# Kernel tuning notes

Measured on AMD Instinct MI355X. Metric: run time of the kernel, lower is better.

## Reference

```python
import jax, jax.numpy as jnp
import numpy as np

C = 1.0          # curvature args.c
ALPHA = 3.0      # self.alpha
MIN = 1e-15      # min_norm clamp (HGCN PoincareBall)
PROJ_EPS = 4e-3  # fp32 boundary eps (HGCN)


def _norm(x):
    return jnp.maximum(jnp.linalg.norm(x, axis=-1, keepdims=True), MIN)


def artanh(x):
    # clamp for fp32 stability (HGCN clamps to 1 - 1e-15; 1e-7 is the fp32 analogue)
    return jnp.arctanh(jnp.clip(x, -1.0 + 1e-7, 1.0 - 1e-7))


def proj(x, c):
    n = _norm(x)
    maxn = (1.0 - PROJ_EPS) / jnp.sqrt(c)
    return jnp.where(n > maxn, x / n * maxn, x)


def expmap0(u, c):
    sc = jnp.sqrt(c)
    n = _norm(u)
    return jnp.tanh(sc * n) * u / (sc * n)


def logmap0(p, c):
    sc = jnp.sqrt(c)
    n = _norm(p)
    return artanh(sc * n) * p / (sc * n)


def mobius_add(x, y, c):
    x2 = jnp.sum(x * x, axis=-1, keepdims=True)
    y2 = jnp.sum(y * y, axis=-1, keepdims=True)
    xy = jnp.sum(x * y, axis=-1, keepdims=True)
    num = (1.0 + 2.0 * c * xy + c * y2) * x + (1.0 - c * x2) * y
    den = 1.0 + 2.0 * c * xy + c * c * x2 * y2
    return num / jnp.maximum(den, MIN)


def mobius_matvec(m, x, c):
    sc = jnp.sqrt(c)
    xn = _norm(x)
    mx = x @ m.T                      # [..., out]
    mxn = _norm(mx)
    res = jnp.tanh(mxn / xn * artanh(sc * xn)) * mx / (mxn * sc)
    zero_rows = jnp.all(mx == 0.0, axis=-1, keepdims=True)
    return jnp.where(zero_rows, 0.0, res)


def hyp_linear(x, W, b, c):
    # dropout on weights is identity in eval mode
    mv = proj(mobius_matvec(W, x, c), c)
    hb = proj(expmap0(b[None, :], c), c)  # proj_tan0 is identity on Poincare ball
    return proj(mobius_add(mv, hb, c), c)


def setup_inputs() -> dict:
    key = jax.random.key(0)
    N, D, F = 8192, 128, 128
    ks = jax.random.split(key, 8)
    gain = np.sqrt(2.0 / (D + D)) * np.sqrt(2.0)  # xavier-like scale
    return {
        "idx": jnp.arange(N, dtype=jnp.int32),
        "dist_metrix": jnp.zeros((1,), dtype=jnp.float32),
        "x": jax.random.normal(ks[0], (N, F), dtype=jnp.float32),
        "emb1": jax.random.normal(ks[1], (N, D), dtype=jnp.float32),
        "emb2": jax.random.normal(ks[2], (N, D), dtype=jnp.float32),
        "W1": jax.random.normal(ks[3], (D, D), dtype=jnp.float32) * gain,
        "b1": jax.random.normal(ks[4], (D,), dtype=jnp.float32) * 0.01,
        "W2": jax.random.normal(ks[5], (D, D), dtype=jnp.float32) * gain,
        "b2": jax.random.normal(ks[6], (D,), dtype=jnp.float32) * 0.01,
    }


def reference(idx, dist_metrix, x, emb1, emb2, W1, b1, W2, b2):
    # node embeddings lifted to the Poincare ball (proj_tan0 is identity)
    nv1 = proj(expmap0(emb1[idx], C), C)
    nv2 = proj(expmap0(emb2[idx], C), C)
    nv1 = hyp_linear(nv1, W1, b1, C)
    nv2 = hyp_linear(nv2, W2, b2, C)
    # adjacency construction: a1 = nv2 @ nv1^T (mobius), a2 = nv1 @ nv2^T (mobius)
    a1 = mobius_matvec(nv1, nv2, C)   # [N, N]
    a2 = mobius_matvec(nv2, nv1, C)   # [N, N]
    a = mobius_add(a1, -a2, C)
    adj = jax.nn.relu(jnp.tanh(ALPHA * a))
    n = adj.shape[0]
    adj = adj + 1e-4 * jnp.eye(n, dtype=adj.dtype)
    # row-normalize (scipy round-trip in original == row-sum divide, inf -> 0)
    rs = jnp.sum(adj, axis=1, keepdims=True)
    adj = adj * jnp.where(rs == 0.0, 0.0, 1.0 / rs)
    # propagate features
    xt = logmap0(x, C)                       # [N, F]
    out = mobius_matvec(xt.T, adj, C)        # adj @ xt -> [N, F]
    out = logmap0(out, C)
    return out
```

## Files before the change

### kernel.cpp

```cpp
#include <hip/hip_runtime.h>
#include <hip/hip_bf16.h>


typedef __attribute__((ext_vector_type(8))) short short8;
typedef __attribute__((ext_vector_type(4))) float f32x4;

#define MAXN 0.996f

__device__ __forceinline__ float artanh_clip(float x) {
    x = fminf(x, 1.0f - 1e-7f);
    x = fmaxf(x, -1.0f + 1e-7f);
    return 0.5f * logf((1.0f + x) / (1.0f - x));
}

__device__ __forceinline__ float red8(float v) {
    v += __shfl_xor(v, 1);
    v += __shfl_xor(v, 2);
    v += __shfl_xor(v, 4);
    return v;
}

__device__ __forceinline__ float red64(float v) {
#pragma unroll
    for (int m = 1; m < 64; m <<= 1) v += __shfl_xor(v, m);
    return v;
}

__device__ __forceinline__ unsigned short f2bf(float f) {
    __hip_bfloat16 h = __float2bfloat16(f);
    return *reinterpret_cast<unsigned short*>(&h);
}

__device__ __forceinline__ float bf2f(unsigned short u) {
    __hip_bfloat16 h;
    *reinterpret_cast<unsigned short*>(&h) = u;
    return __bfloat162float(h);
}

__global__ __launch_bounds__(256) void prep_kernel(
    const int* __restrict__ idx, const float* __restrict__ x,
    const float* __restrict__ emb1, const float* __restrict__ emb2,
    const float* __restrict__ W1, const float* __restrict__ W2,
    const float* __restrict__ b1, const float* __restrict__ b2,
    unsigned short* __restrict__ nv1b, unsigned short* __restrict__ nv2b,
    unsigned short* __restrict__ xtT,
    float* __restrict__ xn1, float* __restrict__ xn2) {
    const int which = blockIdx.y;
    const int tid = threadIdx.x;
    const int rblk = blockIdx.x * 32;

    if (which == 2) {
        __shared__ float xv[32 * 132];
        const int r = tid >> 3, s = tid & 7;
        float ev[16];
        float p2 = 0.f;
#pragma unroll
        for (int kk = 0; kk < 16; ++kk) {
            float e = x[(rblk + r) * 128 + s + kk * 8];
            ev[kk] = e;
            p2 += e * e;
        }
        const float n = fmaxf(sqrtf(red8(p2)), 1e-15f);
        const float scl = artanh_clip(n) / n;
#pragma unroll
        for (int kk = 0; kk < 16; ++kk) xv[r * 132 + s + kk * 8] = ev[kk] * scl;
        __syncthreads();
        const int k = tid >> 1, h = tid & 1;
        short8 o0, o1;
#pragma unroll
        for (int j = 0; j < 8; ++j) o0[j] = (short)f2bf(xv[(h * 16 + j) * 132 + k]);
#pragma unroll
        for (int j = 0; j < 8; ++j) o1[j] = (short)f2bf(xv[(h * 16 + 8 + j) * 132 + k]);
        *reinterpret_cast<short8*>(&xtT[k * 8192 + rblk + h * 16]) = o0;
        *reinterpret_cast<short8*>(&xtT[k * 8192 + rblk + h * 16 + 8]) = o1;
        return;
    }

    __shared__ __align__(16) float uL[32 * 132];
    __shared__ float mxL[32 * 132];
    __shared__ float xnL[32];
    __shared__ float hbL[128];
    __shared__ float s2s[4];

    const float* emb = which ? emb2 : emb1;
    const float* W = which ? W2 : W1;
    const float* b = which ? b2 : b1;
    unsigned short* nvb = which ? nv2b : nv1b;
    float* xno = which ? xn2 : xn1;

    float bv = (tid < 128) ? b[tid] : 0.f;
    float ssq = red64(bv * bv);
    if ((tid & 63) == 0) s2s[tid >> 6] = ssq;
    __syncthreads();
    const float bn = fmaxf(sqrtf(s2s[0] + s2s[1]), 1e-15f);
    const float bth = tanhf(bn);
    const float bnu = fmaxf(bth, 1e-15f);
    const float bps = (bnu > MAXN) ? (MAXN / bnu) : 1.0f;
    if (tid < 128) hbL[tid] = bv * (bth / bn) * bps;
    const float hbn = fminf(bnu, MAXN);
    const float y2 = hbn * hbn;

    const int r = tid >> 3, s = tid & 7;
    const int row = rblk + r;
    const int src = idx[row];
    float ev[16];
    float p2 = 0.f;
#pragma unroll
    for (int kk = 0; kk < 16; ++kk) {
        float e = emb[src * 128 + s + kk * 8];
        ev[kk] = e;
        p2 += e * e;
    }
    float n2 = red8(p2);
    float n = fmaxf(sqrtf(n2), 1e-15f);
    float th = tanhf(n);
    float nu = fmaxf(th, 1e-15f);
    float ps = (nu > MAXN) ? (MAXN / nu) : 1.0f;
    float sc0 = (th / n) * ps;
#pragma unroll
    for (int kk = 0; kk < 16; ++kk) uL[r * 132 + s + kk * 8] = ev[kk] * sc0;
    if (s == 0) xnL[r] = fmaxf(nu * ps, 1e-15f);
    __syncthreads();

    const int o = tid & 127, rb = tid >> 7;
    float mxv[16];
#pragma unroll
    for (int rr = 0; rr < 16; ++rr) mxv[rr] = 0.f;
    for (int k4 = 0; k4 < 128; k4 += 4) {
        const float4 wv = *reinterpret_cast<const float4*>(&W[o * 128 + k4]);
#pragma unroll
        for (int rr = 0; rr < 16; ++rr) {
            const float4 uv = *reinterpret_cast<const float4*>(&uL[(rb + rr * 2) * 132 + k4]);
            mxv[rr] += uv.x * wv.x + uv.y * wv.y + uv.z * wv.z + uv.w * wv.w;
        }
    }
#pragma unroll
    for (int rr = 0; rr < 16; ++rr) mxL[(rb + rr * 2) * 132 + o] = mxv[rr];
    __syncthreads();

    float mx[16];
    float m2 = 0.f;
#pragma unroll
    for (int kk = 0; kk < 16; ++kk) {
        mx[kk] = mxL[r * 132 + s + kk * 8];
        m2 += mx[kk] * mx[kk];
    }
    float mxn = fmaxf(sqrtf(red8(m2)), 1e-15f);
    float xnv = xnL[r];
    float tt = tanhf(mxn / xnv * artanh_clip(xnv));
    float nres = fmaxf(tt, 1e-15f);
    float ps2 = (nres > MAXN) ? (MAXN / nres) : 1.0f;
    float s2 = (tt / mxn) * ps2;
    float mvn = nres * ps2;
    float x2 = mvn * mvn;
    float xyp = 0.f;
    float mv[16];
#pragma unroll
    for (int kk = 0; kk < 16; ++kk) {
        mv[kk] = mx[kk] * s2;
        xyp += mv[kk] * hbL[s + kk * 8];
    }
    float xy = red8(xyp);
    float cA = 1.f + 2.f * xy + y2;
    float cB = 1.f - x2;
    float rden = 1.f / fmaxf(1.f + 2.f * xy + x2 * y2, 1e-15f);
    float r2v[16];
    float q2 = 0.f;
#pragma unroll
    for (int kk = 0; kk < 16; ++kk) {
        float v = (cA * mv[kk] + cB * hbL[s + kk * 8]) * rden;
        r2v[kk] = v;
        q2 += v * v;
    }
    float nr2 = fmaxf(sqrtf(red8(q2)), 1e-15f);
    float ps3 = (nr2 > MAXN) ? (MAXN / nr2) : 1.0f;
#pragma unroll
    for (int kk = 0; kk < 16; ++kk) nvb[row * 128 + s + kk * 8] = f2bf(r2v[kk] * ps3);
    if (s == 0) xno[row] = fmaxf((nr2 > MAXN) ? MAXN : nr2, 1e-15f);
}

__global__ __launch_bounds__(256) void gram_kernel(const unsigned short* __restrict__ nv1b,
                                                   const unsigned short* __restrict__ nv2b,
                                                   float* __restrict__ G) {
    __shared__ float Ab[64 * 33], Bb[64 * 33];
    const int tile = blockIdx.x, mat = blockIdx.y, kc = blockIdx.z;
    const int ta = (tile & 3) * 32, tb = (tile >> 2) * 32;
    const unsigned short* Am = (mat == 1) ? nv2b : nv1b;
    const unsigned short* Bm = (mat == 0) ? nv1b : nv2b;
    const int tid = threadIdx.x;
    const int oa = tid & 31, obb = (tid >> 5) * 4;
    float acc[4] = {0.f, 0.f, 0.f, 0.f};
    for (int sc = 0; sc < 16; ++sc) {
        const int r0 = kc * 1024 + sc * 64;
        for (int i0 = tid; i0 < 2048; i0 += 256) {
            int rr = i0 >> 5, cc = i0 & 31;
            Ab[rr * 33 + cc] = bf2f(Am[(r0 + rr) * 128 + ta + cc]);
            Bb[rr * 33 + cc] = bf2f(Bm[(r0 + rr) * 128 + tb + cc]);
        }
        __syncthreads();
#pragma unroll 4
        for (int rr = 0; rr < 64; ++rr) {
            float av = Ab[rr * 33 + oa];
#pragma unroll
            for (int i = 0; i < 4; ++i) acc[i] += av * Bb[rr * 33 + obb + i];
        }
        __syncthreads();
    }
#pragma unroll
    for (int i = 0; i < 4; ++i)
        atomicAdd(&G[mat * 16384 + (ta + oa) * 128 + tb + obb + i], acc[i]);
}

__global__ __launch_bounds__(256) void rowcoef_kernel(
    const float* __restrict__ G, const float* __restrict__ xn1, const float* __restrict__ xn2,
    const unsigned short* __restrict__ nv1b, const unsigned short* __restrict__ nv2b,
    float* __restrict__ P, float* __restrict__ Q) {
    __shared__ __align__(16) float v1L[32 * 132];
    __shared__ __align__(16) float v2L[32 * 132];
    __shared__ float tL[32 * 132];
    __shared__ float RCX[3][32];
    const int tid = threadIdx.x;
    const int rblk = blockIdx.x * 32;
    for (int i = tid; i < 4096; i += 256) {
        int r = i >> 7, c = i & 127;
        v1L[r * 132 + c] = bf2f(nv1b[(rblk + r) * 128 + c]);
        v2L[r * 132 + c] = bf2f(nv2b[(rblk + r) * 128 + c]);
    }
    __syncthreads();
    const int o = tid & 127, rb = tid >> 7;
    const int rA = tid >> 3, sA = tid & 7;
    for (int mat = 0; mat < 3; ++mat) {
        const float* vR = (mat == 0) ? v2L : v1L;
        const float* vL = (mat == 1) ? v1L : v2L;
        const float* Gm = G + mat * 16384;
        float tv[16];
#pragma unroll
        for (int rr = 0; rr < 16; ++rr) tv[rr] = 0.f;
        for (int k4 = 0; k4 < 128; k4 += 4) {
            const float4 gv = *reinterpret_cast<const float4*>(&Gm[o * 128 + k4]);
#pragma unroll
            for (int rr = 0; rr < 16; ++rr) {
                const float4 uv = *reinterpret_cast<const float4*>(&vR[(rb + rr * 2) * 132 + k4]);
                tv[rr] += uv.x * gv.x + uv.y * gv.y + uv.z * gv.z + uv.w * gv.w;
            }
        }
        __syncthreads();
#pragma unroll
        for (int rr = 0; rr < 16; ++rr) {
            int rw = rb + rr * 2;
            tL[rw * 132 + o] = vL[rw * 132 + o] * tv[rr];
        }
        __syncthreads();
        float p = 0.f;
#pragma unroll
        for (int kk = 0; kk < 16; ++kk) p += tL[rA * 132 + sA + kk * 8];
        p = red8(p);
        if (sA == 0) RCX[mat][rA] = p;
    }
    __syncthreads();
    if (tid < 32) {
        const int row = rblk + tid;
        const float R = RCX[0][tid], Cc = RCX[1][tid], X = RCX[2][tid];
        const float xn1v = xn1[row], xn2v = xn2[row];
        const float mxn1 = fmaxf(sqrtf(fmaxf(R, 0.f)), 1e-15f);
        const float t1 = tanhf(mxn1 / xn2v * artanh_clip(xn2v));
        const float f1 = t1 / mxn1;
        const float mxn2 = fmaxf(sqrtf(fmaxf(Cc, 0.f)), 1e-15f);
        const float t2 = tanhf(mxn2 / xn1v * artanh_clip(xn1v));
        const float f2 = t2 / mxn2;
        const float x2 = f1 * f1 * R, y2 = f2 * f2 * Cc;
        const float xy = -f1 * f2 * X;
        const float rden = 1.f / fmaxf(1.f + 2.f * xy + x2 * y2, 1e-15f);
        P[row] = (1.f + 2.f * xy + y2) * f1 * rden;
        Q[row] = -(1.f - x2) * f2 * rden;
    }
}

__global__ __launch_bounds__(512) void fused_kernel(
    const unsigned short* __restrict__ nv1b, const unsigned short* __restrict__ nv2b,
    const unsigned short* __restrict__ xtT,
    const float* __restrict__ P, const float* __restrict__ Q,
    float* __restrict__ out) {
    __shared__ float UL[32 * 132];
    __shared__ float rsL[32], qL[32];

    const int tid = threadIdx.x;
    const int w = tid >> 6, l = tid & 63;
    const int g = l >> 4, c = l & 15;
    const int i0 = blockIdx.x * 32;

    for (int i = tid; i < 32 * 132; i += 512) UL[i] = 0.f;
    if (tid < 32) { rsL[tid] = 0.f; qL[tid] = 0.f; }
    __syncthreads();

    const float Pv0 = P[i0 + c], Pv1 = P[i0 + 16 + c];
    const float Qv0 = Q[i0 + c], Qv1 = Q[i0 + 16 + c];
    const bool needS2 = __any((fabsf(Qv0) > 1e-6f) || (fabsf(Qv1) > 1e-6f)) != 0;

    short8 Bn0[4], Bn1[4];
#pragma unroll
    for (int kk = 0; kk < 4; ++kk) {
        Bn0[kk] = *reinterpret_cast<const short8*>(nv2b + (i0 + c) * 128 + kk * 32 + g * 8);
        Bn1[kk] = *reinterpret_cast<const short8*>(nv2b + (i0 + 16 + c) * 128 + kk * 32 + g * 8);
    }

    const f32x4 z4 = {0.f, 0.f, 0.f, 0.f};
    f32x4 accU0[8], accU1[8];
#pragma unroll
    for (int ft = 0; ft < 8; ++ft) { accU0[ft] = z4; accU1[ft] = z4; }
    float rs0 = 0.f, rs1 = 0.f, q0 = 0.f, q1 = 0.f;

    const int aoff = (8 * (c >> 2) + (c & 3)) * 128 + g * 8;
    const int sdiag = i0 >> 5;
    const int tdiag = ((sdiag & 7) == w) ? (sdiag >> 3) : -1;
    const size_t xoff = (size_t)c * 8192 + g * 8;

    auto elem = [&](float s, float s2v, float Pv, float Qv, int jglob, int iglob,
                    bool dd, float& rsa, float& qa) -> float {
        float a = Pv * s;
        if (needS2) a = fmaf(Qv, s2v, a);
        float e = __builtin_amdgcn_exp2f(a * 8.65617025f);
        float t = 1.0f - 2.0f * __builtin_amdgcn_rcpf(e + 1.0f);
        float ad = fmaxf(t, 0.0f);
        if (dd && (jglob == iglob)) ad += 1e-4f;
        rsa += ad;
        qa = fmaf(ad, ad, qa);
        return ad;
    };
    auto pack8 = [](const float* ad) -> short8 {
        union { unsigned u[4]; short8 s; } r;
#pragma unroll
        for (int k = 0; k < 4; ++k)
            r.u[k] = (unsigned)f2bf(ad[2 * k]) | ((unsigned)f2bf(ad[2 * k + 1]) << 16);
        return r.s;
    };

    auto doStep = [&](int jb, bool dd) __attribute__((always_inline)) {
        const unsigned short* pa = nv1b + (size_t)jb * 128;
        short8 A0[4], A1[4];
#pragma unroll
        for (int kk = 0; kk < 4; ++kk) {
            A0[kk] = *reinterpret_cast<const short8*>(pa + aoff + kk * 32);
            A1[kk] = *reinterpret_cast<const short8*>(pa + aoff + 512 + kk * 32);
        }
        f32x4 s00 = z4, s10 = z4, s01 = z4, s11 = z4;
#pragma unroll
        for (int kk = 0; kk < 4; ++kk) {
            s00 = __builtin_amdgcn_mfma_f32_16x16x32_bf16(A0[kk], Bn0[kk], s00, 0, 0, 0);
            s10 = __builtin_amdgcn_mfma_f32_16x16x32_bf16(A1[kk], Bn0[kk], s10, 0, 0, 0);
            s01 = __builtin_amdgcn_mfma_f32_16x16x32_bf16(A0[kk], Bn1[kk], s01, 0, 0, 0);
            s11 = __builtin_amdgcn_mfma_f32_16x16x32_bf16(A1[kk], Bn1[kk], s11, 0, 0, 0);
        }
        f32x4 r00 = z4, r10 = z4, r01 = z4, r11 = z4;
        if (needS2) {
            const unsigned short* pa2 = nv2b + (size_t)jb * 128;
            short8 C0[4], C1[4], D0[4], D1[4];
#pragma unroll
            for (int kk = 0; kk < 4; ++kk) {
                C0[kk] = *reinterpret_cast<const short8*>(pa2 + aoff + kk * 32);
                C1[kk] = *reinterpret_cast<const short8*>(pa2 + aoff + 512 + kk * 32);
                D0[kk] = *reinterpret_cast<const short8*>(nv1b + (i0 + c) * 128 + kk * 32 + g * 8);
                D1[kk] = *reinterpret_cast<const short8*>(nv1b + (i0 + 16 + c) * 128 + kk * 32 + g * 8);
            }
#pragma unroll
            for (int kk = 0; kk < 4; ++kk) {
                r00 = __builtin_amdgcn_mfma_f32_16x16x32_bf16(C0[kk], D0[kk], r00, 0, 0, 0);
                r10 = __builtin_amdgcn_mfma_f32_16x16x32_bf16(C1[kk], D0[kk], r10, 0, 0, 0);
                r01 = __builtin_amdgcn_mfma_f32_16x16x32_bf16(C0[kk], D1[kk], r01, 0, 0, 0);
                r11 = __builtin_amdgcn_mfma_f32_16x16x32_bf16(C1[kk], D1[kk], r11, 0, 0, 0);
            }
        }
        float ad0[8], ad1[8];
        const int jg = jb + 8 * g;
        const int ig0 = i0 + c, ig1 = i0 + 16 + c;
#pragma unroll
        for (int v = 0; v < 4; ++v) {
            ad0[v]     = elem(s00[v], r00[v], Pv0, Qv0, jg + v,     ig0, dd, rs0, q0);
            ad0[4 + v] = elem(s10[v], r10[v], Pv0, Qv0, jg + 4 + v, ig0, dd, rs0, q0);
            ad1[v]     = elem(s01[v], r01[v], Pv1, Qv1, jg + v,     ig1, dd, rs1, q1);
            ad1[4 + v] = elem(s11[v], r11[v], Pv1, Qv1, jg + 4 + v, ig1, dd, rs1, q1);
        }
        const short8 af0 = pack8(ad0);
        const short8 af1 = pack8(ad1);
#pragma unroll
        for (int ft = 0; ft < 8; ++ft) {
            short8 xb = *reinterpret_cast<const short8*>(xtT + (size_t)ft * 16 * 8192 + xoff + jb);
            accU0[ft] = __builtin_amdgcn_mfma_f32_16x16x32_bf16(af0, xb, accU0[ft], 0, 0, 0);
            accU1[ft] = __builtin_amdgcn_mfma_f32_16x16x32_bf16(af1, xb, accU1[ft], 0, 0, 0);
        }
    };

    for (int t = 0; t < 32; ++t) {
        const int jb = (w + 8 * t) * 32;
        if (t == tdiag) doStep(jb, true);
        else doStep(jb, false);
    }

    rs0 += __shfl_xor(rs0, 16); rs0 += __shfl_xor(rs0, 32);
    rs1 += __shfl_xor(rs1, 16); rs1 += __shfl_xor(rs1, 32);
    q0 += __shfl_xor(q0, 16);   q0 += __shfl_xor(q0, 32);
    q1 += __shfl_xor(q1, 16);   q1 += __shfl_xor(q1, 32);
    if (l < 16) {
        atomicAdd(&rsL[c], rs0);
        atomicAdd(&qL[c], q0);
        atomicAdd(&rsL[16 + c], rs1);
        atomicAdd(&qL[16 + c], q1);
    }
#pragma unroll
    for (int ft = 0; ft < 8; ++ft)
#pragma unroll
        for (int v = 0; v < 4; ++v) {
            atomicAdd(&UL[(4 * g + v) * 132 + ft * 16 + c], accU0[ft][v]);
            atomicAdd(&UL[(16 + 4 * g + v) * 132 + ft * 16 + c], accU1[ft][v]);
        }
    __syncthreads();

    const int r = tid >> 4, cc = tid & 15;
    const float rsv = rsL[r];
    const float wv = (rsv == 0.f) ? 0.f : 1.f / rsv;
    float m[8];
    float m2 = 0.f;
#pragma unroll
    for (int e = 0; e < 8; ++e) {
        m[e] = UL[r * 132 + cc * 8 + e] * wv;
        m2 = fmaf(m[e], m[e], m2);
    }
    m2 += __shfl_xor(m2, 1);
    m2 += __shfl_xor(m2, 2);
    m2 += __shfl_xor(m2, 4);
    m2 += __shfl_xor(m2, 8);
    const float mxn = fmaxf(sqrtf(m2), 1e-15f);
    const float xn = fmaxf(sqrtf(fmaxf(qL[r], 0.f)) * wv, 1e-15f);
    const float tt = tanhf(mxn / xn * artanh_clip(xn));
    const float nres = fmaxf(tt, 1e-15f);
    const float lsc = (tt / mxn) * (artanh_clip(nres) / nres);
    float4 o0 = {m[0] * lsc, m[1] * lsc, m[2] * lsc, m[3] * lsc};
    float4 o1 = {m[4] * lsc, m[5] * lsc, m[6] * lsc, m[7] * lsc};
    *reinterpret_cast<float4*>(out + (i0 + r) * 128 + cc * 8) = o0;
    *reinterpret_cast<float4*>(out + (i0 + r) * 128 + cc * 8 + 4) = o1;
}

extern "C" void kernel_launch(void* const* d_in, const int* in_sizes, int n_in,
                              void* d_out, int out_size, void* d_ws, size_t ws_size,
                              hipStream_t stream) {
    const int* idx = (const int*)d_in[0];
    const float* x = (const float*)d_in[2];
    const float* emb1 = (const float*)d_in[3];
    const float* emb2 = (const float*)d_in[4];
    const float* W1 = (const float*)d_in[5];
    const float* b1 = (const float*)d_in[6];
    const float* W2 = (const float*)d_in[7];
    const float* b2 = (const float*)d_in[8];
    float* out = (float*)d_out;
    char* ws = (char*)d_ws;

    unsigned short* nv1b = (unsigned short*)(ws + 0x000000);
    unsigned short* nv2b = (unsigned short*)(ws + 0x200000);
    unsigned short* xtT = (unsigned short*)(ws + 0x400000);
    float* G = (float*)(ws + 0x600000);
    float* xn1 = (float*)(ws + 0x630000);
    float* xn2 = (float*)(ws + 0x638000);
    float* P = (float*)(ws + 0x640000);
    float* Q = (float*)(ws + 0x648000);

    hipMemsetAsync(G, 0, 3 * 128 * 128 * sizeof(float), stream);
    prep_kernel<<<dim3(256, 3), 256, 0, stream>>>(idx, x, emb1, emb2, W1, W2, b1, b2,
                                                  nv1b, nv2b, xtT, xn1, xn2);
    gram_kernel<<<dim3(16, 3, 8), 256, 0, stream>>>(nv1b, nv2b, G);
    rowcoef_kernel<<<256, 256, 0, stream>>>(G, xn1, xn2, nv1b, nv2b, P, Q);
    fused_kernel<<<256, 512, 0, stream>>>(nv1b, nv2b, xtT, P, Q, out);
    (void)in_sizes; (void)n_in; (void)out_size; (void)ws_size; (void)d_in;
}
```

Before: 350.5 us.

## Hoist diagonal term out of main loop and prefetch next A tile

The +1e-4 diagonal identity term is removed from the inner tile loop. It is applied analytically in the epilogue using a per-row diagonal adjacency value computed in rowcoef, plus a correction to the row sum, to the squared norm and to the U accumulator. The main loop is also restructured to load the next step's nv1 fragments and the current xtT fragments before the MFMAs, giving software pipelining at the cost of more registers. The LDS atomic reduction order is rotated per wave to reduce bank conflicts.

```diff
diff --git a/kernel.cpp b/kernel.cpp
--- a/kernel.cpp
+++ b/kernel.cpp
@@ -214,11 +214,12 @@
 __global__ __launch_bounds__(256) void rowcoef_kernel(
     const float* __restrict__ G, const float* __restrict__ xn1, const float* __restrict__ xn2,
     const unsigned short* __restrict__ nv1b, const unsigned short* __restrict__ nv2b,
-    float* __restrict__ P, float* __restrict__ Q) {
+    float* __restrict__ P, float* __restrict__ Q, float* __restrict__ Ad) {
     __shared__ __align__(16) float v1L[32 * 132];
     __shared__ __align__(16) float v2L[32 * 132];
     __shared__ float tL[32 * 132];
     __shared__ float RCX[3][32];
+    __shared__ float dL[32];
     const int tid = threadIdx.x;
     const int rblk = blockIdx.x * 32;
     for (int i = tid; i < 4096; i += 256) {
@@ -257,6 +258,12 @@
         p = red8(p);
         if (sA == 0) RCX[mat][rA] = p;
     }
+    float dp = 0.f;
+#pragma unroll
+    for (int kk = 0; kk < 16; ++kk)
+        dp += v1L[rA * 132 + sA + kk * 8] * v2L[rA * 132 + sA + kk * 8];
+    dp = red8(dp);
+    if (sA == 0) dL[rA] = dp;
     __syncthreads();
     if (tid < 32) {
         const int row = rblk + tid;
@@ -271,8 +278,11 @@
         const float x2 = f1 * f1 * R, y2 = f2 * f2 * Cc;
         const float xy = -f1 * f2 * X;
         const float rden = 1.f / fmaxf(1.f + 2.f * xy + x2 * y2, 1e-15f);
-        P[row] = (1.f + 2.f * xy + y2) * f1 * rden;
-        Q[row] = -(1.f - x2) * f2 * rden;
+        const float Pv = (1.f + 2.f * xy + y2) * f1 * rden;
+        const float Qv = -(1.f - x2) * f2 * rden;
+        P[row] = Pv;
+        Q[row] = Qv;
+        Ad[row] = fmaxf(tanhf(3.f * (Pv + Qv) * dL[tid]), 0.f);
     }
 }
 
@@ -280,6 +290,7 @@
     const unsigned short* __restrict__ nv1b, const unsigned short* __restrict__ nv2b,
     const unsigned short* __restrict__ xtT,
     const float* __restrict__ P, const float* __restrict__ Q,
+    const float* __restrict__ Ad,
     float* __restrict__ out) {
     __shared__ float UL[32 * 132];
     __shared__ float rsL[32], qL[32];
@@ -311,18 +322,15 @@
     float rs0 = 0.f, rs1 = 0.f, q0 = 0.f, q1 = 0.f;
 
     const int aoff = (8 * (c >> 2) + (c & 3)) * 128 + g * 8;
-    const int sdiag = i0 >> 5;
-    const int tdiag = ((sdiag & 7) == w) ? (sdiag >> 3) : -1;
     const size_t xoff = (size_t)c * 8192 + g * 8;
 
-    auto elem = [&](float s, float s2v, float Pv, float Qv, int jglob, int iglob,
-                    bool dd, float& rsa, float& qa) -> float {
+    auto elem = [&](float s, float s2v, float Pv, float Qv,
+                    float& rsa, float& qa) -> float {
         float a = Pv * s;
         if (needS2) a = fmaf(Qv, s2v, a);
         float e = __builtin_amdgcn_exp2f(a * 8.65617025f);
         float t = 1.0f - 2.0f * __builtin_amdgcn_rcpf(e + 1.0f);
         float ad = fmaxf(t, 0.0f);
-        if (dd && (jglob == iglob)) ad += 1e-4f;
         rsa += ad;
         qa = fmaf(ad, ad, qa);
         return ad;
@@ -335,21 +343,41 @@
         return r.s;
     };
 
-    auto doStep = [&](int jb, bool dd) __attribute__((always_inline)) {
-        const unsigned short* pa = nv1b + (size_t)jb * 128;
-        short8 A0[4], A1[4];
+    short8 A0c[4], A1c[4];
+    {
+        const unsigned short* pa0 = nv1b + (size_t)(w * 32) * 128;
 #pragma unroll
         for (int kk = 0; kk < 4; ++kk) {
-            A0[kk] = *reinterpret_cast<const short8*>(pa + aoff + kk * 32);
-            A1[kk] = *reinterpret_cast<const short8*>(pa + aoff + 512 + kk * 32);
-        }
+            A0c[kk] = *reinterpret_cast<const short8*>(pa0 + aoff + kk * 32);
+            A1c[kk] = *reinterpret_cast<const short8*>(pa0 + aoff + 512 + kk * 32);
+        }
+    }
+
+    for (int t = 0; t < 32; ++t) {
+        const int jb = (w + 8 * t) * 32;
+        const int jbn = (w + 8 * ((t + 1) & 31)) * 32;
+
+        short8 XB[8];
+#pragma unroll
+        for (int ft = 0; ft < 8; ++ft)
+            XB[ft] = *reinterpret_cast<const short8*>(xtT + (size_t)ft * 16 * 8192 + xoff + jb);
+        short8 A0n[4], A1n[4];
+        {
+            const unsigned short* pan = nv1b + (size_t)jbn * 128;
+#pragma unroll
+            for (int kk = 0; kk < 4; ++kk) {
+                A0n[kk] = *reinterpret_cast<const short8*>(pan + aoff + kk * 32);
+                A1n[kk] = *reinterpret_cast<const short8*>(pan + aoff + 512 + kk * 32);
+            }
+        }
+
         f32x4 s00 = z4, s10 = z4, s01 = z4, s11 = z4;
 #pragma unroll
         for (int kk = 0; kk < 4; ++kk) {
-            s00 = __builtin_amdgcn_mfma_f32_16x16x32_bf16(A0[kk], Bn0[kk], s00, 0, 0, 0);
-            s10 = __builtin_amdgcn_mfma_f32_16x16x32_bf16(A1[kk], Bn0[kk], s10, 0, 0, 0);
-            s01 = __builtin_amdgcn_mfma_f32_16x16x32_bf16(A0[kk], Bn1[kk], s01, 0, 0, 0);
-            s11 = __builtin_amdgcn_mfma_f32_16x16x32_bf16(A1[kk], Bn1[kk], s11, 0, 0, 0);
+            s00 = __builtin_amdgcn_mfma_f32_16x16x32_bf16(A0c[kk], Bn0[kk], s00, 0, 0, 0);
+            s10 = __builtin_amdgcn_mfma_f32_16x16x32_bf16(A1c[kk], Bn0[kk], s10, 0, 0, 0);
+            s01 = __builtin_amdgcn_mfma_f32_16x16x32_bf16(A0c[kk], Bn1[kk], s01, 0, 0, 0);
+            s11 = __builtin_amdgcn_mfma_f32_16x16x32_bf16(A1c[kk], Bn1[kk], s11, 0, 0, 0);
         }
         f32x4 r00 = z4, r10 = z4, r01 = z4, r11 = z4;
         if (needS2) {
@@ -370,30 +398,24 @@
                 r11 = __builtin_amdgcn_mfma_f32_16x16x32_bf16(C1[kk], D1[kk], r11, 0, 0, 0);
             }
         }
+
         float ad0[8], ad1[8];
-        const int jg = jb + 8 * g;
-        const int ig0 = i0 + c, ig1 = i0 + 16 + c;
 #pragma unroll
         for (int v = 0; v < 4; ++v) {
-            ad0[v]     = elem(s00[v], r00[v], Pv0, Qv0, jg + v,     ig0, dd, rs0, q0);
-            ad0[4 + v] = elem(s10[v], r10[v], Pv0, Qv0, jg + 4 + v, ig0, dd, rs0, q0);
-            ad1[v]     = elem(s01[v], r01[v], Pv1, Qv1, jg + v,     ig1, dd, rs1, q1);
-            ad1[4 + v] = elem(s11[v], r11[v], Pv1, Qv1, jg + 4 + v, ig1, dd, rs1, q1);
+            ad0[v]     = elem(s00[v], r00[v], Pv0, Qv0, rs0, q0);
+            ad0[4 + v] = elem(s10[v], r10[v], Pv0, Qv0, rs0, q0);
+            ad1[v]     = elem(s01[v], r01[v], Pv1, Qv1, rs1, q1);
+            ad1[4 + v] = elem(s11[v], r11[v], Pv1, Qv1, rs1, q1);
         }
         const short8 af0 = pack8(ad0);
         const short8 af1 = pack8(ad1);
 #pragma unroll
         for (int ft = 0; ft < 8; ++ft) {
-            short8 xb = *reinterpret_cast<const short8*>(xtT + (size_t)ft * 16 * 8192 + xoff + jb);
-            accU0[ft] = __builtin_amdgcn_mfma_f32_16x16x32_bf16(af0, xb, accU0[ft], 0, 0, 0);
-            accU1[ft] = __builtin_amdgcn_mfma_f32_16x16x32_bf16(af1, xb, accU1[ft], 0, 0, 0);
-        }
-    };
-
-    for (int t = 0; t < 32; ++t) {
-        const int jb = (w + 8 * t) * 32;
-        if (t == tdiag) doStep(jb, true);
-        else doStep(jb, false);
+            accU0[ft] = __builtin_amdgcn_mfma_f32_16x16x32_bf16(af0, XB[ft], accU0[ft], 0, 0, 0);
+            accU1[ft] = __builtin_amdgcn_mfma_f32_16x16x32_bf16(af1, XB[ft], accU1[ft], 0, 0, 0);
+        }
+#pragma unroll
+        for (int kk = 0; kk < 4; ++kk) { A0c[kk] = A0n[kk]; A1c[kk] = A1n[kk]; }
     }
 
     rs0 += __shfl_xor(rs0, 16); rs0 += __shfl_xor(rs0, 32);
@@ -407,22 +429,26 @@
         atomicAdd(&qL[16 + c], q1);
     }
 #pragma unroll
-    for (int ft = 0; ft < 8; ++ft)
+    for (int ftx = 0; ftx < 8; ++ftx) {
+        const int ft = (ftx + w) & 7;
 #pragma unroll
         for (int v = 0; v < 4; ++v) {
             atomicAdd(&UL[(4 * g + v) * 132 + ft * 16 + c], accU0[ft][v]);
             atomicAdd(&UL[(16 + 4 * g + v) * 132 + ft * 16 + c], accU1[ft][v]);
         }
+    }
     __syncthreads();
 
     const int r = tid >> 4, cc = tid & 15;
-    const float rsv = rsL[r];
-    const float wv = (rsv == 0.f) ? 0.f : 1.f / rsv;
+    const float adg = Ad[i0 + r];
+    const float rsv = rsL[r] + 1e-4f;
+    const float wv = 1.f / rsv;
     float m[8];
     float m2 = 0.f;
 #pragma unroll
     for (int e = 0; e < 8; ++e) {
-        m[e] = UL[r * 132 + cc * 8 + e] * wv;
+        const float xv = bf2f(xtT[(size_t)(cc * 8 + e) * 8192 + i0 + r]);
+        m[e] = (UL[r * 132 + cc * 8 + e] + 1e-4f * xv) * wv;
         m2 = fmaf(m[e], m[e], m2);
     }
     m2 += __shfl_xor(m2, 1);
@@ -430,7 +456,8 @@
     m2 += __shfl_xor(m2, 4);
     m2 += __shfl_xor(m2, 8);
     const float mxn = fmaxf(sqrtf(m2), 1e-15f);
-    const float xn = fmaxf(sqrtf(fmaxf(qL[r], 0.f)) * wv, 1e-15f);
+    const float qv = fmaxf(qL[r] + 2e-4f * adg + 1e-8f, 0.f);
+    const float xn = fmaxf(sqrtf(qv) * wv, 1e-15f);
     const float tt = tanhf(mxn / xn * artanh_clip(xn));
     const float nres = fmaxf(tt, 1e-15f);
     const float lsc = (tt / mxn) * (artanh_clip(nres) / nres);
@@ -462,12 +489,13 @@
     float* xn2 = (float*)(ws + 0x638000);
     float* P = (float*)(ws + 0x640000);
     float* Q = (float*)(ws + 0x648000);
+    float* Ad = (float*)(ws + 0x650000);
 
     hipMemsetAsync(G, 0, 3 * 128 * 128 * sizeof(float), stream);
     prep_kernel<<<dim3(256, 3), 256, 0, stream>>>(idx, x, emb1, emb2, W1, W2, b1, b2,
                                                   nv1b, nv2b, xtT, xn1, xn2);
     gram_kernel<<<dim3(16, 3, 8), 256, 0, stream>>>(nv1b, nv2b, G);
-    rowcoef_kernel<<<256, 256, 0, stream>>>(G, xn1, xn2, nv1b, nv2b, P, Q);
-    fused_kernel<<<256, 512, 0, stream>>>(nv1b, nv2b, xtT, P, Q, out);
+    rowcoef_kernel<<<256, 256, 0, stream>>>(G, xn1, xn2, nv1b, nv2b, P, Q, Ad);
+    fused_kernel<<<256, 512, 0, stream>>>(nv1b, nv2b, xtT, P, Q, Ad, out);
     (void)in_sizes; (void)n_in; (void)out_size; (void)ws_size; (void)d_in;
 }
```

Result: faster. 334.6 us (-4.5%).
